# Optimization experiments

Measured on AMD Instinct MI355X. Metric: run time of the kernel, lower is better.

The kernel has to match this reference:

```python
import jax, jax.numpy as jnp
import numpy as np

DIM = 1024
AUX = 3
B, S = 32, 1024
ENC_D = DIM * AUX  # 3072


def setup_inputs() -> dict:
    key = jax.random.key(0)
    ks = jax.random.split(key, 5)
    sc1 = 1.0 / np.sqrt(DIM * (AUX + 1))
    sc3 = 1.0 / np.sqrt(ENC_D)
    return {
        "hidden_state": jax.random.normal(ks[0], (B, DIM), jnp.float32),
        "encoder_outputs": jax.random.normal(ks[1], (B, S, ENC_D), jnp.float32),
        "W1": jax.random.normal(ks[2], (DIM, DIM * (AUX + 1)), jnp.float32) * sc1,
        "b1": jnp.zeros((DIM,), jnp.float32),
        "w2": jax.random.normal(ks[3], (1, DIM), jnp.float32) * (1.0 / np.sqrt(DIM)),
        "W3": jax.random.normal(ks[4], (DIM, ENC_D), jnp.float32) * sc3,
        "b3": jnp.zeros((DIM,), jnp.float32),
    }


def reference(hidden_state, encoder_outputs, W1, b1, w2, W3, b3):
    # hidden_state: (B, dim); encoder_outputs: (B, S, dim*aux)
    Bsz, Slen, _ = encoder_outputs.shape
    h = jnp.broadcast_to(hidden_state[:, None, :], (Bsz, Slen, hidden_state.shape[-1]))
    inputs = jnp.concatenate([encoder_outputs, h], axis=2)  # (B, S, dim*(aux+1))
    # score MLP: tanh(linear1) -> linear2 (no bias)
    hidden = jnp.tanh(jnp.einsum('bsf,df->bsd', inputs, W1) + b1)  # (B, S, dim)
    e = jnp.einsum('bsd,od->bso', hidden, w2)[..., 0]  # (B, S)
    alpha = jax.nn.softmax(e, axis=1)
    context = jnp.einsum('bs,bsf->bf', alpha, encoder_outputs)  # (B, dim*aux)
    return jnp.einsum('bf,df->bd', context, W3) + b3  # (B, dim)
```

## Files before the change

kernel.cpp:

```cpp
#include <hip/hip_runtime.h>
#include <hip/hip_bf16.h>


typedef float          fx4 __attribute__((ext_vector_type(4)));
typedef short          sv8 __attribute__((ext_vector_type(8)));
typedef unsigned short uv4 __attribute__((ext_vector_type(4)));
typedef unsigned int   ui4 __attribute__((ext_vector_type(4)));

__device__ __forceinline__ unsigned short f2bf(float x) {
  unsigned u = __float_as_uint(x);
  return (unsigned short)((u + 0x7FFFu + ((u >> 16) & 1u)) >> 16);
}
__device__ __forceinline__ unsigned cvtpk(float lo, float hi) {
  unsigned r;
  asm("v_cvt_pk_bf16_f32 %0, %1, %2" : "=v"(r) : "v"(lo), "v"(hi));
  return r;
}
__device__ __forceinline__ ui4 pack8(fx4 a, fx4 b) {
  ui4 v;
  v[0] = cvtpk(a[0], a[1]); v[1] = cvtpk(a[2], a[3]);
  v[2] = cvtpk(b[0], b[1]); v[3] = cvtpk(b[2], b[3]);
  return v;
}

#define GLD(srcp, dstp)                                               \
  __builtin_amdgcn_global_load_lds(                                   \
      (const __attribute__((address_space(1))) void*)(srcp),          \
      (__attribute__((address_space(3))) void*)(dstp), 16, 0, 0)

__global__ void convw1_kernel(const float* __restrict__ W1, unsigned short* __restrict__ W1a) {
  int id = blockIdx.x * 256 + threadIdx.x;
  int d = id / 768, fi = id - d * 768;
  fx4 v = ((const fx4*)W1)[d * 1024 + fi];
  uv4 r; r[0] = f2bf(v[0]); r[1] = f2bf(v[1]); r[2] = f2bf(v[2]); r[3] = f2bf(v[3]);
  ((uv4*)W1a)[d * 768 + fi] = r;
}

__global__ void convenc_kernel(const float* __restrict__ enc, unsigned short* __restrict__ ebf) {
  int id = blockIdx.x * 256 + threadIdx.x;
  fx4 a = ((const fx4*)enc)[2 * id];
  fx4 b = ((const fx4*)enc)[2 * id + 1];
  ((ui4*)ebf)[id] = pack8(a, b);
}

__global__ void hbias_kernel(const float* __restrict__ hs, const float* __restrict__ W1,
                             const float* __restrict__ b1, float* __restrict__ hb) {
  int idx = (blockIdx.x << 2) + (threadIdx.x >> 6);
  int lane = threadIdx.x & 63;
  int b = idx >> 10, d = idx & 1023;
  const fx4* hv = (const fx4*)hs;
  const fx4* wv = (const fx4*)W1;
  float s = 0.f;
#pragma unroll
  for (int i = 0; i < 4; ++i) {
    int k4 = lane + (i << 6);
    fx4 h = hv[(b << 8) + k4];
    fx4 w = wv[d * 1024 + 768 + k4];
    s += h[0] * w[0] + h[1] * w[1] + h[2] * w[2] + h[3] * w[3];
  }
#pragma unroll
  for (int off = 32; off; off >>= 1) s += __shfl_xor(s, off);
  if (lane == 0) hb[idx] = s + b1[d];
}

__global__ __launch_bounds__(256, 2)
void gemm8(const unsigned short* __restrict__ Ag,
           const unsigned short* __restrict__ Bg,
           const float* __restrict__ hb,
           const float* __restrict__ w2,
           float* __restrict__ pe) {
  __shared__ __align__(16) unsigned short Ab[2][8192];
  __shared__ __align__(16) unsigned short Bb[2][8192];

  const int t = threadIdx.x, lane = t & 63, wid = t >> 6;
  const int wm = wid >> 1, wn = wid & 1;

  const int bid = blockIdx.x;
  const int lg = ((bid & 7) << 8) | (bid >> 3);
  const int mt = lg >> 3, nt = lg & 7;
  const int row0 = mt << 7, col0 = nt << 7;

  const int l3 = lane >> 3, l7 = lane & 7;
  const unsigned short* asrc = Ag + (size_t)(row0 + wid * 32 + l3) * 3072 + ((l7 ^ l3) << 3);
  const unsigned short* bsrc = Bg + (size_t)(col0 + wid * 32 + l3) * 3072 + ((l7 ^ l3) << 3);
  const int dstb = wid << 11;

  const int r15 = lane & 15, qv = lane >> 4;
  const int aB = (wm * 64 + r15) << 6;
  const int bB = (wn * 64 + r15) << 6;
  const int s0 = (qv ^ (r15 & 7)) << 3;
  const int s1 = ((qv + 4) ^ (r15 & 7)) << 3;

  fx4 acc[4][4] = {};

#define ST_B(BN, kt, g) GLD(bsrc + (g) * 24576 + (kt) * 64, &Bb[BN][dstb + ((g) << 9)])
#define ST_A(AN, kt, g) GLD(asrc + (g) * 24576 + (kt) * 64, &Ab[AN][dstb + ((g) << 9)])

#define PHASE(P, KH)                                                  \
  { sv8 af[4], bfv[4];                                                \
    const int sx = (KH) ? s1 : s0;                                    \
    _Pragma("unroll")                                                 \
    for (int mi = 0; mi < 4; ++mi)                                    \
      af[mi] = *(const sv8*)&Ab[P][aB + (mi << 10) + sx];             \
    _Pragma("unroll")                                                 \
    for (int ni = 0; ni < 4; ++ni)                                    \
      bfv[ni] = *(const sv8*)&Bb[P][bB + (ni << 10) + sx];            \
    __builtin_amdgcn_s_setprio(1);                                    \
    _Pragma("unroll")                                                 \
    for (int mi = 0; mi < 4; ++mi)                                    \
      _Pragma("unroll")                                               \
      for (int ni = 0; ni < 4; ++ni)                                  \
        acc[mi][ni] = __builtin_amdgcn_mfma_f32_16x16x32_bf16(        \
            af[mi], bfv[ni], acc[mi][ni], 0, 0, 0);                   \
    __builtin_amdgcn_s_setprio(0);                                    \
  }

#define TILE(kt, P)                                                   \
  { if ((kt) < 47) {                                                  \
      ST_B(P ^ 1, (kt) + 1, 0); ST_B(P ^ 1, (kt) + 1, 1);             \
      ST_B(P ^ 1, (kt) + 1, 2); ST_B(P ^ 1, (kt) + 1, 3);             \
      ST_A(P ^ 1, (kt) + 1, 0); ST_A(P ^ 1, (kt) + 1, 1);             \
      ST_A(P ^ 1, (kt) + 1, 2); ST_A(P ^ 1, (kt) + 1, 3);             \
    }                                                                 \
    PHASE(P, 0)                                                       \
    PHASE(P, 1)                                                       \
    asm volatile("s_waitcnt lgkmcnt(0)" ::: "memory");                \
    asm volatile("s_waitcnt vmcnt(0)" ::: "memory");                  \
    __builtin_amdgcn_s_barrier(); }

  ST_B(0, 0, 0); ST_B(0, 0, 1); ST_B(0, 0, 2); ST_B(0, 0, 3);
  ST_A(0, 0, 0); ST_A(0, 0, 1); ST_A(0, 0, 2); ST_A(0, 0, 3);
  asm volatile("s_waitcnt vmcnt(0)" ::: "memory");
  __builtin_amdgcn_s_barrier();

  for (int it = 0; it < 24; ++it) {
    TILE(2 * it, 0)
    TILE(2 * it + 1, 1)
  }

  const int b = row0 >> 10;
  float w2v[4], hbv[4];
#pragma unroll
  for (int ni = 0; ni < 4; ++ni) {
    int c = col0 + wn * 64 + ni * 16 + r15;
    w2v[ni] = w2[c];
    hbv[ni] = hb[(b << 10) + c];
  }
#pragma unroll
  for (int mi = 0; mi < 4; ++mi) {
#pragma unroll
    for (int j = 0; j < 4; ++j) {
      float pz = 0.f;
#pragma unroll
      for (int ni = 0; ni < 4; ++ni)
        pz += tanhf(acc[mi][ni][j] + hbv[ni]) * w2v[ni];
      pz += __shfl_xor(pz, 1); pz += __shfl_xor(pz, 2);
      pz += __shfl_xor(pz, 4); pz += __shfl_xor(pz, 8);
      if (r15 == 0) {
        int row = row0 + wm * 64 + mi * 16 + (qv << 2) + j;
        pe[(row << 4) + (nt << 1) + wn] = pz;
      }
    }
  }
#undef ST_A
#undef ST_B
#undef PHASE
#undef TILE
}

__global__ __launch_bounds__(512, 2)
void gemm2(const float* __restrict__ enc,
           const unsigned short* __restrict__ W1a,
           const float* __restrict__ hb,
           const float* __restrict__ w2,
           float* __restrict__ pe) {
  __shared__ __align__(16) unsigned short As[2][10240];
  __shared__ __align__(16) unsigned short Bs[2][8192];
  const int t = threadIdx.x;
  const int lane = t & 63, wid = t >> 6;
  const int wm = wid >> 2, wn = wid & 3;
  const int bid = blockIdx.x;
  const int lg = ((bid & 7) << 6) | (bid >> 3);
  const int mt = lg >> 2, ntile = lg & 3;
  const int row0 = mt << 8;
  const int col0 = ntile << 8;
  const fx4* encv = (const fx4*)enc;
  const int ar = t >> 1, ah = t & 1;
  const int agb = (row0 + ar) * 768 + ah * 4;
  const int awb = ar * 40 + ah * 16;
  const int l3 = lane >> 3, l7 = lane & 7;
  const int pre = l7 ^ l3;
  const unsigned short* bsrc0 =
      W1a + (size_t)(col0 + wid * 32 + 2 * l3 + (pre >> 2)) * 3072 + (pre & 3) * 8;
  const unsigned short* bsrc1 = bsrc0 + (size_t)16 * 3072;
  const int bdst0 = (wid * 16) * 64;
  const int bdst1 = (wid * 16 + 8) * 64;
  const int r15 = lane & 15, qv = lane >> 4;
  const int aro = (wm * 128 + r15) * 40 + qv * 8;
  const int cb = wn * 64 + r15;
  const int bro = (cb >> 1) * 64 + (((((cb & 1) << 2) + qv) ^ ((cb >> 1) & 7)) << 3);
  fx4 acc[8][4] = {};
  fx4 pa[2][4];
#define A_LOAD(s, kt) { _Pragma("unroll") for (int j = 0; j < 4; ++j) pa[s][j] = encv[agb + (kt) * 8 + j]; }
#define A_WRITE(s, buf) { *(ui4*)&As[buf][awb] = pack8(pa[s][0], pa[s][1]); \
                          *(ui4*)&As[buf][awb + 8] = pack8(pa[s][2], pa[s][3]); }
#define B_ISSUE(buf, kt) { GLD(bsrc0 + (kt) * 32, &Bs[buf][bdst0]); \
                           GLD(bsrc1 + (kt) * 32, &Bs[buf][bdst1]); }
#define COMPUTE(p)                                                    \
  { sv8 af[8], bfv[4];                                                \
    _Pragma("unroll")                                                 \
    for (int mi = 0; mi < 8; ++mi) af[mi] = *(const sv8*)&As[p][aro + mi * 640]; \
    _Pragma("unroll")                                                 \
    for (int ni = 0; ni < 4; ++ni) bfv[ni] = *(const sv8*)&Bs[p][bro + ni * 512]; \
    _Pragma("unroll")                                                 \
    for (int mi = 0; mi < 8; ++mi)                                    \
      _Pragma("unroll")                                               \
      for (int ni = 0; ni < 4; ++ni)                                  \
        acc[mi][ni] = __builtin_amdgcn_mfma_f32_16x16x32_bf16(af[mi], bfv[ni], acc[mi][ni], 0, 0, 0); }
#define ITER(kt, p)                                                   \
  { COMPUTE(p)                                                        \
    if ((kt) < 95) { A_WRITE(p ^ 1, p ^ 1) }                          \
    if ((kt) < 93) { A_LOAD(p ^ 1, (kt) + 3) }                        \
    __builtin_amdgcn_s_barrier();                                     \
    if ((kt) < 94) {                                                  \
      B_ISSUE(p, (kt) + 2)                                            \
      asm volatile("s_waitcnt vmcnt(6)" ::: "memory");                \
    } else if ((kt) == 94) {                                          \
      asm volatile("s_waitcnt vmcnt(0)" ::: "memory");                \
    }                                                                 \
    asm volatile("s_waitcnt lgkmcnt(0)" ::: "memory");                \
    __builtin_amdgcn_s_barrier(); }
  A_LOAD(0, 0)
  A_LOAD(1, 1)
  B_ISSUE(0, 0)
  A_WRITE(0, 0)
  B_ISSUE(1, 1)
  A_LOAD(0, 2)
  asm volatile("s_waitcnt vmcnt(6)" ::: "memory");
  asm volatile("s_waitcnt lgkmcnt(0)" ::: "memory");
  __builtin_amdgcn_s_barrier();
  for (int kt2 = 0; kt2 < 48; ++kt2) {
    const int kt = kt2 * 2;
    ITER(kt, 0)
    ITER(kt + 1, 1)
  }
  const int b = row0 >> 10;
  float w2v[4], hbv[4];
#pragma unroll
  for (int ni = 0; ni < 4; ++ni) {
    int c = col0 + wn * 64 + ni * 16 + r15;
    w2v[ni] = w2[c];
    hbv[ni] = hb[(b << 10) + c];
  }
#pragma unroll
  for (int mi = 0; mi < 8; ++mi) {
#pragma unroll
    for (int j = 0; j < 4; ++j) {
      float pz = 0.f;
#pragma unroll
      for (int ni = 0; ni < 4; ++ni)
        pz += tanhf(acc[mi][ni][j] + hbv[ni]) * w2v[ni];
      pz += __shfl_xor(pz, 1); pz += __shfl_xor(pz, 2);
      pz += __shfl_xor(pz, 4); pz += __shfl_xor(pz, 8);
      if (r15 == 0) {
        int row = row0 + wm * 128 + mi * 16 + (qv << 2) + j;
        pe[(row << 4) + (ntile << 2) + wn] = pz;
      }
    }
  }
#undef A_LOAD
#undef A_WRITE
#undef B_ISSUE
#undef COMPUTE
#undef ITER
}

__global__ void softmax_kernel(const float* __restrict__ pe, float* __restrict__ alpha) {
  int b = blockIdx.x, t = threadIdx.x;
  int lane = t & 63, wid = t >> 6;
  float ev[4];
#pragma unroll
  for (int r = 0; r < 4; ++r) {
    int s = t + r * 256;
    const float* p = pe + ((b << 10) + s) * 16;
    float sum = 0.f;
#pragma unroll
    for (int i = 0; i < 16; ++i) sum += p[i];
    ev[r] = sum;
  }
  float m = fmaxf(fmaxf(ev[0], ev[1]), fmaxf(ev[2], ev[3]));
#pragma unroll
  for (int off = 32; off; off >>= 1) m = fmaxf(m, __shfl_xor(m, off));
  __shared__ float red[8];
  if (lane == 0) red[wid] = m;
  __syncthreads();
  m = fmaxf(fmaxf(red[0], red[1]), fmaxf(red[2], red[3]));
  float p4[4], ls = 0.f;
#pragma unroll
  for (int r = 0; r < 4; ++r) { p4[r] = expf(ev[r] - m); ls += p4[r]; }
#pragma unroll
  for (int off = 32; off; off >>= 1) ls += __shfl_xor(ls, off);
  if (lane == 0) red[4 + wid] = ls;
  __syncthreads();
  float inv = 1.0f / (red[4] + red[5] + red[6] + red[7]);
#pragma unroll
  for (int r = 0; r < 4; ++r) alpha[(b << 10) + t + r * 256] = p4[r] * inv;
}

__global__ void ctxpart_bf_kernel(const unsigned short* __restrict__ ebf,
                                  const float* __restrict__ alpha,
                                  float* __restrict__ part) {
  int bid = blockIdx.x, b = bid >> 4, sc = bid & 15;
  int t = threadIdx.x;
  __shared__ float sal[64];
  if (t < 64) sal[t] = alpha[(b << 10) + (sc << 6) + t];
  __syncthreads();
  const ui4* ev = (const ui4*)ebf;
  float a8[8] = {};
  int base = ((b << 10) + (sc << 6)) * 384;
  for (int si = 0; si < 64; ++si) {
    float a = sal[si];
    ui4 v = ev[base + si * 384 + t];
#pragma unroll
    for (int j = 0; j < 4; ++j) {
      unsigned u = v[j];
      a8[2 * j]     += a * __uint_as_float(u << 16);
      a8[2 * j + 1] += a * __uint_as_float(u & 0xFFFF0000u);
    }
  }
  fx4* pp = (fx4*)part;
  int pb = ((b << 4) + sc) * 768 + t * 2;
  fx4 o0 = {a8[0], a8[1], a8[2], a8[3]};
  fx4 o1 = {a8[4], a8[5], a8[6], a8[7]};
  pp[pb] = o0; pp[pb + 1] = o1;
}

__global__ void ctxpart_kernel(const float* __restrict__ enc, const float* __restrict__ alpha,
                               float* __restrict__ part) {
  int bid = blockIdx.x, b = bid >> 4, sc = bid & 15;
  int t = threadIdx.x;
  __shared__ float sal[64];
  if (t < 64) sal[t] = alpha[(b << 10) + (sc << 6) + t];
  __syncthreads();
  const fx4* ev = (const fx4*)enc;
  fx4 a0 = {}, a1 = {}, a2 = {};
  int base = ((b << 10) + (sc << 6)) * 768;
  for (int si = 0; si < 64; ++si) {
    float a = sal[si];
    const fx4* rp = ev + base + si * 768;
    a0 += a * rp[t];
    a1 += a * rp[256 + t];
    a2 += a * rp[512 + t];
  }
  fx4* pp = (fx4*)part;
  int pb = ((b << 4) + sc) * 768;
  pp[pb + t] = a0; pp[pb + 256 + t] = a1; pp[pb + 512 + t] = a2;
}

__global__ void ctxreduce_kernel(const float* __restrict__ part, float* __restrict__ ctx) {
  int j = blockIdx.x * 256 + threadIdx.x;
  int b = j / 768, fi = j - b * 768;
  const fx4* pp = (const fx4*)part;
  fx4 s = {};
#pragma unroll
  for (int i = 0; i < 16; ++i) s += pp[((b << 4) + i) * 768 + fi];
  ((fx4*)ctx)[b * 768 + fi] = s;
}

__global__ void final_kernel(const float* __restrict__ ctx, const float* __restrict__ W3,
                             const float* __restrict__ b3, float* __restrict__ out) {
  int idx = (blockIdx.x << 2) + (threadIdx.x >> 6);
  int lane = threadIdx.x & 63;
  int b = idx >> 10, d = idx & 1023;
  const fx4* cv = (const fx4*)ctx;
  const fx4* wv = (const fx4*)W3;
  float s = 0.f;
#pragma unroll
  for (int i = 0; i < 12; ++i) {
    int f4 = lane + (i << 6);
    fx4 c = cv[b * 768 + f4];
    fx4 w = wv[d * 768 + f4];
    s += c[0] * w[0] + c[1] * w[1] + c[2] * w[2] + c[3] * w[3];
  }
#pragma unroll
  for (int off = 32; off; off >>= 1) s += __shfl_xor(s, off);
  if (lane == 0) out[idx] = s + b3[d];
}

extern "C" void kernel_launch(void* const* d_in, const int* in_sizes, int n_in,
                              void* d_out, int out_size, void* d_ws, size_t ws_size,
                              hipStream_t stream) {
  const float* hs  = (const float*)d_in[0];
  const float* enc = (const float*)d_in[1];
  const float* W1  = (const float*)d_in[2];
  const float* b1  = (const float*)d_in[3];
  const float* w2  = (const float*)d_in[4];
  const float* W3  = (const float*)d_in[5];
  const float* b3  = (const float*)d_in[6];
  float* out = (float*)d_out;
  char* ws = (char*)d_ws;

  const size_t NEED_A = 216662016ULL;

  if (ws_size >= NEED_A) {
    unsigned short* ebf = (unsigned short*)(ws);
    unsigned short* W1a = (unsigned short*)(ws + 201326592);
    float* pe    = (float*)(ws + 207618048);
    float* alpha = (float*)(ws + 209715200);
    float* hb    = (float*)(ws + 209846272);
    float* ctx   = (float*)(ws + 209977344);
    float* part  = (float*)(ws + 210370560);

    convw1_kernel<<<3072, 256, 0, stream>>>(W1, W1a);
    convenc_kernel<<<49152, 256, 0, stream>>>(enc, ebf);
    hbias_kernel<<<8192, 256, 0, stream>>>(hs, W1, b1, hb);
    gemm8<<<2048, 256, 0, stream>>>(ebf, W1a, hb, w2, pe);
    softmax_kernel<<<32, 256, 0, stream>>>(pe, alpha);
    ctxpart_bf_kernel<<<512, 384, 0, stream>>>(ebf, alpha, part);
    ctxreduce_kernel<<<96, 256, 0, stream>>>(part, ctx);
    final_kernel<<<8192, 256, 0, stream>>>(ctx, W3, b3, out);
  } else {
    unsigned short* W1a = (unsigned short*)(ws);
    float* pe    = (float*)(ws + 6291456);
    float* alpha = (float*)(ws + 8388608);
    float* hb    = (float*)(ws + 8519680);
    float* ctx   = (float*)(ws + 8650752);
    float* part  = (float*)(ws + 9043968);

    convw1_kernel<<<3072, 256, 0, stream>>>(W1, W1a);
    hbias_kernel<<<8192, 256, 0, stream>>>(hs, W1, b1, hb);
    gemm2<<<512, 512, 0, stream>>>(enc, W1a, hb, w2, pe);
    softmax_kernel<<<32, 256, 0, stream>>>(pe, alpha);
    ctxpart_kernel<<<512, 256, 0, stream>>>(enc, alpha, part);
    ctxreduce_kernel<<<96, 256, 0, stream>>>(part, ctx);
    final_kernel<<<8192, 256, 0, stream>>>(ctx, W3, b3, out);
  }
}
```

Baseline: 451.1 us.

## Halve GEMM K-tile to 32 and raise occupancy to five blocks per CU

The main bf16 MFMA GEMM now stages a K-slice of 32 instead of 64 per iteration, halving LDS per block (16 KB to 8 KB double-buffered). The launch bound goes from 2 to 5 blocks per CU to gain occupancy. The LDS layout and swizzle are reworked so that two rows share a 64-element LDS line, and the per-iteration setprio hints are dropped. In exchange there are twice as many barriers and waitcnt stalls per tile, and the tighter register budget could spill the 64-float accumulator.

After: 480.3 us. 6.5% more time.

```diff
diff --git a/kernel.cpp b/kernel.cpp
--- a/kernel.cpp
+++ b/kernel.cpp
@@ -63,14 +63,14 @@
   if (lane == 0) hb[idx] = s + b1[d];
 }
 
-__global__ __launch_bounds__(256, 2)
-void gemm8(const unsigned short* __restrict__ Ag,
-           const unsigned short* __restrict__ Bg,
-           const float* __restrict__ hb,
-           const float* __restrict__ w2,
-           float* __restrict__ pe) {
-  __shared__ __align__(16) unsigned short Ab[2][8192];
-  __shared__ __align__(16) unsigned short Bb[2][8192];
+__global__ __launch_bounds__(256, 5)
+void gemmM97(const unsigned short* __restrict__ Ag,
+             const unsigned short* __restrict__ Bg,
+             const float* __restrict__ hb,
+             const float* __restrict__ w2,
+             float* __restrict__ pe) {
+  __shared__ __align__(16) unsigned short Ab[2][4096];
+  __shared__ __align__(16) unsigned short Bb[2][4096];
 
   const int t = threadIdx.x, lane = t & 63, wid = t >> 6;
   const int wm = wid >> 1, wn = wid & 1;
@@ -81,59 +81,51 @@
   const int row0 = mt << 7, col0 = nt << 7;
 
   const int l3 = lane >> 3, l7 = lane & 7;
-  const unsigned short* asrc = Ag + (size_t)(row0 + wid * 32 + l3) * 3072 + ((l7 ^ l3) << 3);
-  const unsigned short* bsrc = Bg + (size_t)(col0 + wid * 32 + l3) * 3072 + ((l7 ^ l3) << 3);
-  const int dstb = wid << 11;
+  const int pre = l7 ^ l3;
+  const unsigned short* asrc0 =
+      Ag + (size_t)(row0 + wid * 32 + 2 * l3 + (pre >> 2)) * 3072 + (pre & 3) * 8;
+  const unsigned short* asrc1 = asrc0 + (size_t)16 * 3072;
+  const unsigned short* bsrc0 =
+      Bg + (size_t)(col0 + wid * 32 + 2 * l3 + (pre >> 2)) * 3072 + (pre & 3) * 8;
+  const unsigned short* bsrc1 = bsrc0 + (size_t)16 * 3072;
+  const int dst0 = wid * 1024;
+  const int dst1 = wid * 1024 + 512;
 
   const int r15 = lane & 15, qv = lane >> 4;
-  const int aB = (wm * 64 + r15) << 6;
-  const int bB = (wn * 64 + r15) << 6;
-  const int s0 = (qv ^ (r15 & 7)) << 3;
-  const int s1 = ((qv + 4) ^ (r15 & 7)) << 3;
+  const int sS = ((((r15 & 1) << 2) + qv) ^ ((r15 >> 1) & 7)) << 3;
+  const int aro = wm * 2048 + (r15 >> 1) * 64 + sS;
+  const int bro = wn * 2048 + (r15 >> 1) * 64 + sS;
 
   fx4 acc[4][4] = {};
 
-#define ST_B(BN, kt, g) GLD(bsrc + (g) * 24576 + (kt) * 64, &Bb[BN][dstb + ((g) << 9)])
-#define ST_A(AN, kt, g) GLD(asrc + (g) * 24576 + (kt) * 64, &Ab[AN][dstb + ((g) << 9)])
-
-#define PHASE(P, KH)                                                  \
-  { sv8 af[4], bfv[4];                                                \
-    const int sx = (KH) ? s1 : s0;                                    \
-    _Pragma("unroll")                                                 \
-    for (int mi = 0; mi < 4; ++mi)                                    \
-      af[mi] = *(const sv8*)&Ab[P][aB + (mi << 10) + sx];             \
-    _Pragma("unroll")                                                 \
-    for (int ni = 0; ni < 4; ++ni)                                    \
-      bfv[ni] = *(const sv8*)&Bb[P][bB + (ni << 10) + sx];            \
-    __builtin_amdgcn_s_setprio(1);                                    \
+#define STAGE(P, kt)                                                  \
+  { GLD(asrc0 + (kt) * 32, &Ab[P][dst0]);                             \
+    GLD(asrc1 + (kt) * 32, &Ab[P][dst1]);                             \
+    GLD(bsrc0 + (kt) * 32, &Bb[P][dst0]);                             \
+    GLD(bsrc1 + (kt) * 32, &Bb[P][dst1]); }
+
+#define TILE(kt, P)                                                   \
+  { if ((kt) < 95) { STAGE(P ^ 1, (kt) + 1) }                         \
+    sv8 af[4], bfv[4];                                                \
+    _Pragma("unroll")                                                 \
+    for (int mi = 0; mi < 4; ++mi) af[mi] = *(const sv8*)&Ab[P][aro + mi * 512]; \
+    _Pragma("unroll")                                                 \
+    for (int ni = 0; ni < 4; ++ni) bfv[ni] = *(const sv8*)&Bb[P][bro + ni * 512]; \
     _Pragma("unroll")                                                 \
     for (int mi = 0; mi < 4; ++mi)                                    \
       _Pragma("unroll")                                               \
       for (int ni = 0; ni < 4; ++ni)                                  \
         acc[mi][ni] = __builtin_amdgcn_mfma_f32_16x16x32_bf16(        \
             af[mi], bfv[ni], acc[mi][ni], 0, 0, 0);                   \
-    __builtin_amdgcn_s_setprio(0);                                    \
-  }
-
-#define TILE(kt, P)                                                   \
-  { if ((kt) < 47) {                                                  \
-      ST_B(P ^ 1, (kt) + 1, 0); ST_B(P ^ 1, (kt) + 1, 1);             \
-      ST_B(P ^ 1, (kt) + 1, 2); ST_B(P ^ 1, (kt) + 1, 3);             \
-      ST_A(P ^ 1, (kt) + 1, 0); ST_A(P ^ 1, (kt) + 1, 1);             \
-      ST_A(P ^ 1, (kt) + 1, 2); ST_A(P ^ 1, (kt) + 1, 3);             \
-    }                                                                 \
-    PHASE(P, 0)                                                       \
-    PHASE(P, 1)                                                       \
     asm volatile("s_waitcnt lgkmcnt(0)" ::: "memory");                \
     asm volatile("s_waitcnt vmcnt(0)" ::: "memory");                  \
     __builtin_amdgcn_s_barrier(); }
 
-  ST_B(0, 0, 0); ST_B(0, 0, 1); ST_B(0, 0, 2); ST_B(0, 0, 3);
-  ST_A(0, 0, 0); ST_A(0, 0, 1); ST_A(0, 0, 2); ST_A(0, 0, 3);
+  STAGE(0, 0)
   asm volatile("s_waitcnt vmcnt(0)" ::: "memory");
   __builtin_amdgcn_s_barrier();
 
-  for (int it = 0; it < 24; ++it) {
+  for (int it = 0; it < 48; ++it) {
     TILE(2 * it, 0)
     TILE(2 * it + 1, 1)
   }
@@ -162,9 +154,7 @@
       }
     }
   }
-#undef ST_A
-#undef ST_B
-#undef PHASE
+#undef STAGE
 #undef TILE
 }
 
@@ -414,7 +404,7 @@
     convw1_kernel<<<3072, 256, 0, stream>>>(W1, W1a);
     convenc_kernel<<<49152, 256, 0, stream>>>(enc, ebf);
     hbias_kernel<<<8192, 256, 0, stream>>>(hs, W1, b1, hb);
-    gemm8<<<2048, 256, 0, stream>>>(ebf, W1a, hb, w2, pe);
+    gemmM97<<<2048, 256, 0, stream>>>(ebf, W1a, hb, w2, pe);
     softmax_kernel<<<32, 256, 0, stream>>>(pe, alpha);
     ctxpart_bf_kernel<<<512, 384, 0, stream>>>(ebf, alpha, part);
     ctxreduce_kernel<<<96, 256, 0, stream>>>(part, ctx);
```
